# Optimization experiments

Measured on AMD Instinct MI355X. Metric: run time of the kernel, lower is better.

Reference implementation:

```python
import jax, jax.numpy as jnp
import numpy as np

# SofthebbArgs constants (rate, adaptive=True, p, dot_uw=False, temp)
RATE = 1e-3
TEMP = 1.0
P = 0.5


def negate_non_maximal(t):
    # keep the per-row max entry, negate all others
    idx = jnp.argmax(t, axis=-1)                      # [B]
    mask = idx[:, None] == jnp.arange(t.shape[-1])    # [B, OUT]
    return jnp.where(mask, t, -t)


def setup_inputs() -> dict:
    key = jax.random.key(0)
    k1, k2 = jax.random.split(key, 2)
    B, IN, OUT = 8192, 1024, 1024
    x = jax.random.normal(k1, (B, IN), dtype=jnp.float32)
    # xavier_normal_ with gain=1: std = sqrt(2/(fan_in+fan_out))
    W = jax.random.normal(k2, (OUT, IN), dtype=jnp.float32) * (2.0 / (IN + OUT)) ** 0.5
    b = jnp.zeros((OUT,), dtype=jnp.float32)
    return {"x": x, "W": W, "b": b}


def reference(x, W, b):
    # --- HebbianLinear.forward (act = Identity) ---
    u = x @ W.T + b                                   # [B, OUT]
    y = u
    # --- softhebb: y = softmax(y / temp), then _hebb with dot_uw=False ---
    ysm = jax.nn.softmax(y / TEMP, axis=1)
    yn = negate_non_maximal(ysm)                      # [B, OUT]
    Bn = x.shape[0]
    # _hebb materializes dw[b,o,i] = yn[b,o]*(x[b,i] - u[b,o]*W[o,i]) then means over b.
    # Algebraically fused (no [B,OUT,IN] intermediate):
    #   step[o,i] = (yn^T x)[o,i]/B - mean_b(yn[b,o]*u[b,o]) * W[o,i]
    step = (yn.T @ x) / Bn - jnp.mean(yn * u, axis=0)[:, None] * W  # [OUT, IN]
    # adaptive per-row rate: rate * |1 - ||W_row||_2|^p
    diff = jnp.abs(1.0 - jnp.linalg.norm(W, axis=1))  # [OUT]
    rate = RATE * diff ** P
    return rate[:, None] * step                       # [OUT, IN]
```

## Files before the change

kernel.cpp:

```cpp
#include <hip/hip_runtime.h>

#define BATCH 8192
#define INF_  1024
#define OUTF  1024
#define INV_B (1.0f/8192.0f)
#define RATE_C 1e-3f
#define SPLITZ 8

typedef __bf16 bf16x8 __attribute__((ext_vector_type(8)));
typedef float  f32x4  __attribute__((ext_vector_type(4)));
typedef const __attribute__((address_space(1))) unsigned int* gas_t;
typedef __attribute__((address_space(3))) unsigned int* las_t;

static __device__ __forceinline__ unsigned short f2bf(float f) {
  unsigned int u = __float_as_uint(f);
  u += 0x7fffu + ((u >> 16) & 1u);
  return (unsigned short)(u >> 16);
}

__global__ __launch_bounds__(256) void k_convert(
    const float* __restrict__ x, unsigned short* __restrict__ xb,
    unsigned short* __restrict__ xT, const float* __restrict__ W,
    unsigned short* __restrict__ Wb, float* __restrict__ rate,
    float* __restrict__ svec) {
  const int t = threadIdx.x;
  if (blockIdx.x >= 2048) {
    __shared__ float red[256];
    const int o = blockIdx.x - 2048;
    float4 v = *(const float4*)&W[(size_t)o * INF_ + t * 4];
    ushort4 h;
    h.x = f2bf(v.x); h.y = f2bf(v.y); h.z = f2bf(v.z); h.w = f2bf(v.w);
    *(ushort4*)&Wb[(size_t)o * INF_ + t * 4] = h;
    red[t] = v.x * v.x + v.y * v.y + v.z * v.z + v.w * v.w;
    __syncthreads();
    for (int s = 128; s > 0; s >>= 1) {
      if (t < s) red[t] += red[t + s];
      __syncthreads();
    }
    if (t == 0) {
      float nrm = sqrtf(red[0]);
      rate[o] = RATE_C * sqrtf(fabsf(1.0f - nrm));
      svec[o] = 0.0f;
    }
    return;
  }
  __shared__ unsigned short tl[64][72];
  const int bx = blockIdx.x & 15;
  const int by = blockIdx.x >> 4;
  const int r0 = by * 64;
  const int c0 = bx * 64;
  const int rr = t >> 4;
  const int cc = (t & 15) * 4;
#pragma unroll
  for (int p = 0; p < 4; ++p) {
    int r = p * 16 + rr;
    float4 v = *(const float4*)&x[(size_t)(r0 + r) * INF_ + c0 + cc];
    ushort4 h;
    h.x = f2bf(v.x); h.y = f2bf(v.y); h.z = f2bf(v.z); h.w = f2bf(v.w);
    *(ushort4*)&xb[(size_t)(r0 + r) * INF_ + c0 + cc] = h;
    tl[cc + 0][r] = h.x; tl[cc + 1][r] = h.y;
    tl[cc + 2][r] = h.z; tl[cc + 3][r] = h.w;
  }
  __syncthreads();
#pragma unroll
  for (int p = 0; p < 4; ++p) {
    int c = p * 16 + rr;
    ushort4 w = *(const ushort4*)&tl[c][cc];
    *(ushort4*)&xT[(size_t)(c0 + c) * BATCH + r0 + cc] = w;
  }
}

__global__ __launch_bounds__(256, 2) void k_gemm(
    const unsigned short* __restrict__ A, const unsigned short* __restrict__ B,
    int lda, int ldb, int kChunk, float* __restrict__ C, int ldc,
    const float* __restrict__ bias, int mode) {
  __shared__ unsigned short As[128 * 64];
  __shared__ unsigned short Bs[128 * 64];
  const int t  = threadIdx.x;
  const int id = blockIdx.x;
  int bx, by, bz;
  if (mode == 0) {
    by = (id & 7) | ((id >> 6) << 3);
    bx = (id >> 3) & 7;
    bz = 0;
  } else {
    bz = id & 7;
    by = (id >> 3) & 7;
    bx = id >> 6;
  }
  const int m0   = by * 128;
  const int n0   = bx * 128;
  const int k0   = bz * kChunk;
  const int lane = t & 63;
  const int wave = t >> 6;
  const int sr   = lane >> 3;
  const int scx  = ((lane & 7) ^ sr) * 8;
  const int wm   = (wave >> 1) * 64;
  const int wn   = (wave & 1) * 64;
  const int fm   = lane & 15;
  const int fk   = (lane >> 4) * 8;

  f32x4 acc[4][4] = {};

  const int ldsRow0 = wave * 8;
  const size_t gArow = (size_t)(m0 + ldsRow0 + sr) * lda + scx;
  const size_t gBrow = (size_t)(n0 + ldsRow0 + sr) * ldb + scx;

  for (int ks = 0; ks < kChunk; ks += 64) {
    const int k = k0 + ks;
#pragma unroll
    for (int j = 0; j < 4; ++j) {
      __builtin_amdgcn_global_load_lds(
          (gas_t)&A[gArow + (size_t)j * 32 * lda + k],
          (las_t)&As[(ldsRow0 + j * 32) * 64], 16, 0, 0);
      __builtin_amdgcn_global_load_lds(
          (gas_t)&B[gBrow + (size_t)j * 32 * ldb + k],
          (las_t)&Bs[(ldsRow0 + j * 32) * 64], 16, 0, 0);
    }
    __syncthreads();
#pragma unroll
    for (int kk = 0; kk < 64; kk += 32) {
      bf16x8 af[4], bf[4];
      const int swz = ((((kk + fk) >> 3) ^ (fm & 7)) << 3);
#pragma unroll
      for (int i = 0; i < 4; ++i)
        af[i] = *(const bf16x8*)&As[(wm + i * 16 + fm) * 64 + swz];
#pragma unroll
      for (int i = 0; i < 4; ++i)
        bf[i] = *(const bf16x8*)&Bs[(wn + i * 16 + fm) * 64 + swz];
#pragma unroll
      for (int mt = 0; mt < 4; ++mt)
#pragma unroll
        for (int nt = 0; nt < 4; ++nt)
          acc[mt][nt] = __builtin_amdgcn_mfma_f32_16x16x32_bf16(
              af[mt], bf[nt], acc[mt][nt], 0, 0, 0);
    }
    __syncthreads();
  }

  const int er = (lane >> 4) * 4;
  if (mode == 0) {
#pragma unroll
    for (int nt = 0; nt < 4; ++nt) {
      const int n  = n0 + wn + nt * 16 + fm;
      const float bv = bias[n];
#pragma unroll
      for (int mt = 0; mt < 4; ++mt) {
        const int mb = m0 + wm + mt * 16 + er;
#pragma unroll
        for (int r = 0; r < 4; ++r)
          C[(size_t)(mb + r) * ldc + n] = acc[mt][nt][r] + bv;
      }
    }
  } else {
    float* Cp = C + (size_t)bz * (1024u * 1024u);
#pragma unroll
    for (int nt = 0; nt < 4; ++nt) {
      const int n = n0 + wn + nt * 16 + fm;
#pragma unroll
      for (int mt = 0; mt < 4; ++mt) {
        const int mb = m0 + wm + mt * 16 + er;
#pragma unroll
        for (int r = 0; r < 4; ++r)
          Cp[(size_t)(mb + r) * ldc + n] = acc[mt][nt][r];
      }
    }
  }
}

__global__ __launch_bounds__(256) void k_row_stats(
    const float* __restrict__ u, const float* __restrict__ x,
    const float* __restrict__ W, float* __restrict__ rowmax,
    float* __restrict__ rowinv, int* __restrict__ rowarg) {
  __shared__ int cands[4][32];
  __shared__ int cnt[4];
  const int lane = threadIdx.x & 63;
  const int wave = threadIdx.x >> 6;
  const int b    = blockIdx.x * 4 + wave;

  float a[16];
  const float* up = &u[(size_t)b * OUTF + lane * 16];
#pragma unroll
  for (int j = 0; j < 16; j += 4) {
    float4 v = *(const float4*)&up[j];
    a[j] = v.x; a[j + 1] = v.y; a[j + 2] = v.z; a[j + 3] = v.w;
  }
  float mv = a[0]; int mi = lane * 16;
#pragma unroll
  for (int j = 1; j < 16; ++j)
    if (a[j] > mv) { mv = a[j]; mi = lane * 16 + j; }
#pragma unroll
  for (int off = 1; off < 64; off <<= 1) {
    float ov = __shfl_xor(mv, off);
    int   oi = __shfl_xor(mi, off);
    if (ov > mv || (ov == mv && oi < mi)) { mv = ov; mi = oi; }
  }
  const float M = mv;
  float se = 0.0f;
#pragma unroll
  for (int j = 0; j < 16; ++j) se += __expf(a[j] - M);
#pragma unroll
  for (int off = 1; off < 64; off <<= 1) se += __shfl_xor(se, off);

  const float thr = M - 0.05f;
  int ccount = 0;
  unsigned int cflags = 0;
#pragma unroll
  for (int j = 0; j < 16; ++j)
    if (a[j] >= thr) { cflags |= (1u << j); ++ccount; }
  int tot = ccount;
#pragma unroll
  for (int off = 1; off < 64; off <<= 1) tot += __shfl_xor(tot, off);

  int best = mi;
  if (tot > 1) {
    if (lane == 0) cnt[wave] = 0;
    for (int j = 0; j < 16; ++j)
      if (cflags & (1u << j)) {
        int p = atomicAdd(&cnt[wave], 1);
        if (p < 32) cands[wave][p] = lane * 16 + j;
      }
    int nc = cnt[wave]; if (nc > 32) nc = 32;
    float xr[16];
    const float* xp = &x[(size_t)b * INF_ + lane * 16];
#pragma unroll
    for (int j = 0; j < 16; j += 4) {
      float4 v = *(const float4*)&xp[j];
      xr[j] = v.x; xr[j + 1] = v.y; xr[j + 2] = v.z; xr[j + 3] = v.w;
    }
    float bv = -3.4e38f; int bi = 0x7fffffff;
    for (int c = 0; c < nc; ++c) {
      const int o = cands[wave][c];
      const float* wp = &W[(size_t)o * INF_ + lane * 16];
      float d = 0.0f;
#pragma unroll
      for (int j = 0; j < 16; j += 4) {
        float4 v = *(const float4*)&wp[j];
        d += xr[j] * v.x + xr[j + 1] * v.y + xr[j + 2] * v.z + xr[j + 3] * v.w;
      }
#pragma unroll
      for (int off = 1; off < 64; off <<= 1) d += __shfl_xor(d, off);
      if (d > bv || (d == bv && o < bi)) { bv = d; bi = o; }
    }
    best = bi;
  }
  if (lane == 0) {
    rowmax[b] = M;
    rowinv[b] = 1.0f / se;
    rowarg[b] = best;
  }
}

__global__ __launch_bounds__(256) void k_yn(
    const float* __restrict__ u, const float* __restrict__ rowmax,
    const float* __restrict__ rowinv, const int* __restrict__ rowarg,
    unsigned short* __restrict__ ynT, float* __restrict__ s) {
  __shared__ unsigned short tile[256][72];
  __shared__ float smax[64], sinv[64];
  __shared__ int   sarg[64];
  const int t  = threadIdx.x;
  const int o0 = blockIdx.x * 256;
  const int b0 = blockIdx.y * 64;
  if (t < 64) {
    smax[t] = rowmax[b0 + t];
    sinv[t] = rowinv[b0 + t];
    sarg[t] = rowarg[b0 + t];
  }
  __syncthreads();
  const int o = o0 + t;
  float sacc = 0.0f;
#pragma unroll
  for (int g = 0; g < 8; ++g) {
    uint4 pkv;
    unsigned short* pk = (unsigned short*)&pkv;
#pragma unroll
    for (int j = 0; j < 8; ++j) {
      const int r = g * 8 + j;
      float uu  = u[(size_t)(b0 + r) * OUTF + o];
      float ysm = __expf(uu - smax[r]) * sinv[r];
      float yn  = (o == sarg[r]) ? ysm : -ysm;
      sacc += yn * uu;
      pk[j] = f2bf(yn);
    }
    *(uint4*)&tile[t][g * 8] = pkv;
  }
  atomicAdd(&s[o], sacc);
  __syncthreads();
#pragma unroll
  for (int it = 0; it < 8; ++it) {
    const int row = it * 32 + (t >> 3);
    const int seg = (t & 7) * 8;
    uint4 vv = *(const uint4*)&tile[row][seg];
    *(uint4*)&ynT[(size_t)(o0 + row) * BATCH + b0 + seg] = vv;
  }
}

__global__ __launch_bounds__(256) void k_final(
    const float* __restrict__ Cp, const float* __restrict__ W,
    const float* __restrict__ s, const float* __restrict__ rate,
    float* __restrict__ out) {
  const int g  = blockIdx.x * 256 + threadIdx.x;
  const int i4 = g * 4;
  const int o  = i4 >> 10;
  float4 c = *(const float4*)&Cp[i4];
#pragma unroll
  for (int z = 1; z < SPLITZ; ++z) {
    float4 cz = *(const float4*)&Cp[(size_t)z * (1024u * 1024u) + i4];
    c.x += cz.x; c.y += cz.y; c.z += cz.z; c.w += cz.w;
  }
  float4 w = *(const float4*)&W[i4];
  const float sb = s[o] * INV_B;
  const float rt = rate[o];
  float4 r;
  r.x = rt * (c.x * INV_B - sb * w.x);
  r.y = rt * (c.y * INV_B - sb * w.y);
  r.z = rt * (c.z * INV_B - sb * w.z);
  r.w = rt * (c.w * INV_B - sb * w.w);
  *(float4*)&out[i4] = r;
}

extern "C" void kernel_launch(void* const* d_in, const int* in_sizes, int n_in,
                              void* d_out, int out_size, void* d_ws, size_t ws_size,
                              hipStream_t stream) {
  const float* x    = (const float*)d_in[0];
  const float* W    = (const float*)d_in[1];
  const float* bias = (const float*)d_in[2];
  float* out = (float*)d_out;
  char* ws = (char*)d_ws;

  float*          u    = (float*)(ws + 0);
  unsigned short* xb   = (unsigned short*)(ws + 33554432);
  unsigned short* xT   = (unsigned short*)(ws + 50331648);
  unsigned short* Wb   = (unsigned short*)(ws + 67108864);
  unsigned short* ynT  = (unsigned short*)(ws + 69206016);
  float*          svec = (float*)(ws + 85983232);
  float*          rate = (float*)(ws + 85987328);
  float*          rmax = (float*)(ws + 85991424);
  float*          rinv = (float*)(ws + 86024192);
  int*            rarg = (int*)  (ws + 86056960);

  k_convert<<<dim3(3072), 256, 0, stream>>>(x, xb, xT, W, Wb, rate, svec);
  k_gemm<<<dim3(512), 256, 0, stream>>>(xb, Wb, 1024, 1024, 1024,
                                        u, 1024, bias, 0);
  k_row_stats<<<dim3(2048), 256, 0, stream>>>(u, x, W, rmax, rinv, rarg);
  k_yn<<<dim3(4, 128), 256, 0, stream>>>(u, rmax, rinv, rarg, ynT, svec);
  k_gemm<<<dim3(512), 256, 0, stream>>>(ynT, xT, 8192, 8192,
                                        8192 / SPLITZ, u, 1024,
                                        nullptr, 1);
  k_final<<<dim3(1024), 256, 0, stream>>>(u, W, svec, rate, out);
}
```

Before: 158.8 us.

## Split-K 16 with bf16 partials, deterministic s reduction, packed transpose, occupancy 3

Raises the second GEMM's split-K from 8 to 16 and stores its partial sums as bf16 instead of fp32, which halves the partial-buffer traffic and doubles the grid to 1024 blocks. The atomicAdd for the per-output s vector is replaced by per-batch-tile partials that k_final reduces in shared memory, and k_final now handles one output row per block. The x transpose in k_convert packs two bf16 values per 32-bit LDS word so the xT stores can be 16-byte wide. The GEMM launch bound is raised to 3 waves-per-EU blocks. Rounding the partials to bf16 before summing adds precision error.

Result: no change. 156.9 us (-1.2%).

```diff
diff --git a/kernel.cpp b/kernel.cpp
--- a/kernel.cpp
+++ b/kernel.cpp
@@ -5,7 +5,7 @@
 #define OUTF  1024
 #define INV_B (1.0f/8192.0f)
 #define RATE_C 1e-3f
-#define SPLITZ 8
+#define SPLITZ 16
 
 typedef __bf16 bf16x8 __attribute__((ext_vector_type(8)));
 typedef float  f32x4  __attribute__((ext_vector_type(4)));
@@ -17,12 +17,14 @@
   u += 0x7fffu + ((u >> 16) & 1u);
   return (unsigned short)(u >> 16);
 }
+static __device__ __forceinline__ float bf2f(unsigned short h) {
+  return __uint_as_float(((unsigned int)h) << 16);
+}
 
 __global__ __launch_bounds__(256) void k_convert(
     const float* __restrict__ x, unsigned short* __restrict__ xb,
     unsigned short* __restrict__ xT, const float* __restrict__ W,
-    unsigned short* __restrict__ Wb, float* __restrict__ rate,
-    float* __restrict__ svec) {
+    unsigned short* __restrict__ Wb, float* __restrict__ rate) {
   const int t = threadIdx.x;
   if (blockIdx.x >= 2048) {
     __shared__ float red[256];
@@ -40,37 +42,44 @@
     if (t == 0) {
       float nrm = sqrtf(red[0]);
       rate[o] = RATE_C * sqrtf(fabsf(1.0f - nrm));
-      svec[o] = 0.0f;
     }
     return;
   }
-  __shared__ unsigned short tl[64][72];
+  __shared__ unsigned int t32[64][33];
   const int bx = blockIdx.x & 15;
   const int by = blockIdx.x >> 4;
   const int r0 = by * 64;
   const int c0 = bx * 64;
-  const int rr = t >> 4;
-  const int cc = (t & 15) * 4;
-#pragma unroll
-  for (int p = 0; p < 4; ++p) {
-    int r = p * 16 + rr;
-    float4 v = *(const float4*)&x[(size_t)(r0 + r) * INF_ + c0 + cc];
-    ushort4 h;
-    h.x = f2bf(v.x); h.y = f2bf(v.y); h.z = f2bf(v.z); h.w = f2bf(v.w);
-    *(ushort4*)&xb[(size_t)(r0 + r) * INF_ + c0 + cc] = h;
-    tl[cc + 0][r] = h.x; tl[cc + 1][r] = h.y;
-    tl[cc + 2][r] = h.z; tl[cc + 3][r] = h.w;
+  const int m = t & 15;
+  const int q = t >> 4;
+#pragma unroll
+  for (int p = 0; p < 2; ++p) {
+    const int r2 = p * 16 + q;
+    const int b  = r0 + 2 * r2;
+    float4 v0 = *(const float4*)&x[(size_t)b * INF_ + c0 + 4 * m];
+    float4 v1 = *(const float4*)&x[(size_t)(b + 1) * INF_ + c0 + 4 * m];
+    ushort4 h0, h1;
+    h0.x = f2bf(v0.x); h0.y = f2bf(v0.y); h0.z = f2bf(v0.z); h0.w = f2bf(v0.w);
+    h1.x = f2bf(v1.x); h1.y = f2bf(v1.y); h1.z = f2bf(v1.z); h1.w = f2bf(v1.w);
+    *(ushort4*)&xb[(size_t)b * INF_ + c0 + 4 * m] = h0;
+    *(ushort4*)&xb[(size_t)(b + 1) * INF_ + c0 + 4 * m] = h1;
+    t32[4 * m + 0][r2] = (unsigned int)h0.x | ((unsigned int)h1.x << 16);
+    t32[4 * m + 1][r2] = (unsigned int)h0.y | ((unsigned int)h1.y << 16);
+    t32[4 * m + 2][r2] = (unsigned int)h0.z | ((unsigned int)h1.z << 16);
+    t32[4 * m + 3][r2] = (unsigned int)h0.w | ((unsigned int)h1.w << 16);
   }
   __syncthreads();
-#pragma unroll
-  for (int p = 0; p < 4; ++p) {
-    int c = p * 16 + rr;
-    ushort4 w = *(const ushort4*)&tl[c][cc];
-    *(ushort4*)&xT[(size_t)(c0 + c) * BATCH + r0 + cc] = w;
-  }
-}
-
-__global__ __launch_bounds__(256, 2) void k_gemm(
+  const int c  = t >> 2;
+  const int sg = t & 3;
+  unsigned int vb[8];
+#pragma unroll
+  for (int k = 0; k < 8; ++k) vb[k] = t32[c][sg * 8 + k];
+  unsigned short* dst = &xT[(size_t)(c0 + c) * BATCH + r0 + sg * 16];
+  *(uint4*)&dst[0] = make_uint4(vb[0], vb[1], vb[2], vb[3]);
+  *(uint4*)&dst[8] = make_uint4(vb[4], vb[5], vb[6], vb[7]);
+}
+
+__global__ __launch_bounds__(256, 3) void k_gemm(
     const unsigned short* __restrict__ A, const unsigned short* __restrict__ B,
     int lda, int ldb, int kChunk, float* __restrict__ C, int ldc,
     const float* __restrict__ bias, int mode) {
@@ -84,9 +93,9 @@
     bx = (id >> 3) & 7;
     bz = 0;
   } else {
-    bz = id & 7;
-    by = (id >> 3) & 7;
-    bx = id >> 6;
+    bz = ((id & 7) << 1) | ((id >> 3) & 1);
+    by = (id >> 4) & 7;
+    bx = id >> 7;
   }
   const int m0   = by * 128;
   const int n0   = bx * 128;
@@ -153,7 +162,7 @@
       }
     }
   } else {
-    float* Cp = C + (size_t)bz * (1024u * 1024u);
+    unsigned short* Cp = (unsigned short*)C + (size_t)bz * (1024u * 1024u);
 #pragma unroll
     for (int nt = 0; nt < 4; ++nt) {
       const int n = n0 + wn + nt * 16 + fm;
@@ -162,7 +171,7 @@
         const int mb = m0 + wm + mt * 16 + er;
 #pragma unroll
         for (int r = 0; r < 4; ++r)
-          Cp[(size_t)(mb + r) * ldc + n] = acc[mt][nt][r];
+          Cp[(size_t)(mb + r) * ldc + n] = f2bf(acc[mt][nt][r]);
       }
     }
   }
@@ -254,7 +263,7 @@
 __global__ __launch_bounds__(256) void k_yn(
     const float* __restrict__ u, const float* __restrict__ rowmax,
     const float* __restrict__ rowinv, const int* __restrict__ rowarg,
-    unsigned short* __restrict__ ynT, float* __restrict__ s) {
+    unsigned short* __restrict__ ynT, float* __restrict__ s_part) {
   __shared__ unsigned short tile[256][72];
   __shared__ float smax[64], sinv[64];
   __shared__ int   sarg[64];
@@ -284,7 +293,7 @@
     }
     *(uint4*)&tile[t][g * 8] = pkv;
   }
-  atomicAdd(&s[o], sacc);
+  s_part[(size_t)blockIdx.y * OUTF + o] = sacc;
   __syncthreads();
 #pragma unroll
   for (int it = 0; it < 8; ++it) {
@@ -296,27 +305,35 @@
 }
 
 __global__ __launch_bounds__(256) void k_final(
-    const float* __restrict__ Cp, const float* __restrict__ W,
-    const float* __restrict__ s, const float* __restrict__ rate,
+    const unsigned short* __restrict__ Cp, const float* __restrict__ W,
+    const float* __restrict__ s_part, const float* __restrict__ rate,
     float* __restrict__ out) {
-  const int g  = blockIdx.x * 256 + threadIdx.x;
-  const int i4 = g * 4;
-  const int o  = i4 >> 10;
-  float4 c = *(const float4*)&Cp[i4];
-#pragma unroll
-  for (int z = 1; z < SPLITZ; ++z) {
-    float4 cz = *(const float4*)&Cp[(size_t)z * (1024u * 1024u) + i4];
-    c.x += cz.x; c.y += cz.y; c.z += cz.z; c.w += cz.w;
-  }
-  float4 w = *(const float4*)&W[i4];
-  const float sb = s[o] * INV_B;
+  __shared__ float sred[128];
+  const int t = threadIdx.x;
+  const int o = blockIdx.x;
+  if (t < 128) sred[t] = s_part[(size_t)t * OUTF + o];
+  __syncthreads();
+  for (int s2 = 64; s2 > 0; s2 >>= 1) {
+    if (t < s2) sred[t] += sred[t + s2];
+    __syncthreads();
+  }
+  const float sb = sred[0] * INV_B;
   const float rt = rate[o];
+  const int i0 = t * 4;
+  float cx = 0, cy = 0, cz = 0, cw = 0;
+#pragma unroll
+  for (int z = 0; z < SPLITZ; ++z) {
+    ushort4 h = *(const ushort4*)&Cp[(size_t)z * (1024u * 1024u) +
+                                     (size_t)o * INF_ + i0];
+    cx += bf2f(h.x); cy += bf2f(h.y); cz += bf2f(h.z); cw += bf2f(h.w);
+  }
+  float4 w = *(const float4*)&W[(size_t)o * INF_ + i0];
   float4 r;
-  r.x = rt * (c.x * INV_B - sb * w.x);
-  r.y = rt * (c.y * INV_B - sb * w.y);
-  r.z = rt * (c.z * INV_B - sb * w.z);
-  r.w = rt * (c.w * INV_B - sb * w.w);
-  *(float4*)&out[i4] = r;
+  r.x = rt * (cx * INV_B - sb * w.x);
+  r.y = rt * (cy * INV_B - sb * w.y);
+  r.z = rt * (cz * INV_B - sb * w.z);
+  r.w = rt * (cw * INV_B - sb * w.w);
+  *(float4*)&out[(size_t)o * INF_ + i0] = r;
 }
 
 extern "C" void kernel_launch(void* const* d_in, const int* in_sizes, int n_in,
@@ -328,24 +345,24 @@
   float* out = (float*)d_out;
   char* ws = (char*)d_ws;
 
-  float*          u    = (float*)(ws + 0);
-  unsigned short* xb   = (unsigned short*)(ws + 33554432);
-  unsigned short* xT   = (unsigned short*)(ws + 50331648);
-  unsigned short* Wb   = (unsigned short*)(ws + 67108864);
-  unsigned short* ynT  = (unsigned short*)(ws + 69206016);
-  float*          svec = (float*)(ws + 85983232);
-  float*          rate = (float*)(ws + 85987328);
-  float*          rmax = (float*)(ws + 85991424);
-  float*          rinv = (float*)(ws + 86024192);
-  int*            rarg = (int*)  (ws + 86056960);
-
-  k_convert<<<dim3(3072), 256, 0, stream>>>(x, xb, xT, W, Wb, rate, svec);
+  float*          u     = (float*)(ws + 0);
+  unsigned short* xb    = (unsigned short*)(ws + 33554432);
+  unsigned short* xT    = (unsigned short*)(ws + 50331648);
+  unsigned short* Wb    = (unsigned short*)(ws + 67108864);
+  unsigned short* ynT   = (unsigned short*)(ws + 69206016);
+  float*          rate  = (float*)(ws + 85983232);
+  float*          rmax  = (float*)(ws + 85987328);
+  float*          rinv  = (float*)(ws + 86020096);
+  int*            rarg  = (int*)  (ws + 86052864);
+  float*          spart = (float*)(ws + 86085632);
+
+  k_convert<<<dim3(3072), 256, 0, stream>>>(x, xb, xT, W, Wb, rate);
   k_gemm<<<dim3(512), 256, 0, stream>>>(xb, Wb, 1024, 1024, 1024,
                                         u, 1024, bias, 0);
   k_row_stats<<<dim3(2048), 256, 0, stream>>>(u, x, W, rmax, rinv, rarg);
-  k_yn<<<dim3(4, 128), 256, 0, stream>>>(u, rmax, rinv, rarg, ynT, svec);
-  k_gemm<<<dim3(512), 256, 0, stream>>>(ynT, xT, 8192, 8192,
-                                        8192 / SPLITZ, u, 1024,
-                                        nullptr, 1);
-  k_final<<<dim3(1024), 256, 0, stream>>>(u, W, svec, rate, out);
-}
+  k_yn<<<dim3(4, 128), 256, 0, stream>>>(u, rmax, rinv, rarg, ynT, spart);
+  k_gemm<<<dim3(1024), 256, 0, stream>>>(ynT, xT, 8192, 8192, 512,
+                                         u, 1024, nullptr, 1);
+  k_final<<<dim3(1024), 256, 0, stream>>>((const unsigned short*)u, W, spart,
+                                          rate, out);
+}
```
